# Optimization experiments

Measured on AMD Instinct MI355X. Metric: run time of the kernel, lower is better.

## Reference

```python
import jax, jax.numpy as jnp
import numpy as np

K, D = 4096, 256
BETA, DECAY, EPS = 0.25, 0.99, 1e-05
B = 32768


def setup_inputs() -> dict:
    key = jax.random.key(0)
    k1, k2, k3, k4 = jax.random.split(key, 4)
    return {
        "z_e": jax.random.normal(k1, (B, D), dtype=jnp.float32),
        "codebook": jax.random.normal(k2, (K, D), dtype=jnp.float32),
        "ema_cluster_size": jax.random.uniform(k3, (K,), dtype=jnp.float32),
        "ema_weight": jax.random.normal(k4, (K, D), dtype=jnp.float32),
    }


def reference(z_e, codebook, ema_cluster_size, ema_weight):
    z_e = z_e.astype(jnp.float32)
    # squared L2 distances: ||z||^2 - 2 z.C^T + ||C||^2  (chunking in torch is
    # purely a memory optimization; math is identical)
    e_norm = jnp.sum(z_e * z_e, axis=1, keepdims=True)            # [B,1]
    c_norm = jnp.sum(codebook * codebook, axis=1)                  # [K]
    dists = e_norm - 2.0 * (z_e @ codebook.T) + c_norm[None, :]    # [B,K]
    idx = jnp.argmin(dists, axis=1)                                # [B] int

    z_q = codebook[idx]                                            # [B,d] gather

    # EMA codebook update (no_grad in torch)
    counts = jnp.zeros((K,), jnp.float32).at[idx].add(1.0)         # bincount
    new_cluster = ema_cluster_size * DECAY + counts * (1.0 - DECAY)
    dw = jnp.zeros((K, D), jnp.float32).at[idx].add(z_e)           # index_add_
    new_ema_weight = ema_weight * DECAY + dw * (1.0 - DECAY)
    n = jnp.sum(new_cluster)
    cluster_size = (new_cluster + EPS) / (n + K * EPS) * n
    new_codebook = new_ema_weight / cluster_size[:, None]

    z_q_ste = z_e + jax.lax.stop_gradient(z_q - z_e)
    commit = BETA * jnp.mean((z_e - z_q) ** 2)
    return (z_q_ste, idx, commit, new_codebook, new_cluster, new_ema_weight)
```

## Files before the change

### kernel.cpp

```cpp
#include <hip/hip_runtime.h>

#define KC 4096
#define DD 256
#define BB 32768
#define P_BETA 0.25f
#define P_DECAY 0.99f
#define P_EPS 1e-5f
#define TAU 0.5f
#define CHUNK 32

typedef __attribute__((ext_vector_type(8))) short bf16x8;
typedef __attribute__((ext_vector_type(4))) float f32x4;

static __device__ __forceinline__ unsigned short f2bf(float f) {
    unsigned int u = __float_as_uint(f);
    unsigned int r = (u + 0x7fffu + ((u >> 16) & 1u)) >> 16;
    return (unsigned short)r;
}
static __device__ __forceinline__ void gload_lds16(const void* g, void* s) {
    __builtin_amdgcn_global_load_lds(
        (const __attribute__((address_space(1))) unsigned int*)g,
        (__attribute__((address_space(3))) unsigned int*)s, 16, 0, 0);
}

#define ZBLK (BB * DD / 4 / 256)
#define CBLK (KC * DD / 4 / 256)
__global__ __launch_bounds__(256) void convert_all_kernel(
    const float* __restrict__ z, const float* __restrict__ cb,
    unsigned short* __restrict__ zb, unsigned short* __restrict__ cbb,
    float* __restrict__ cn, int* __restrict__ cnt) {
    const int b = blockIdx.x;
    if (b < ZBLK) {
        int t = b * 256 + threadIdx.x;
        float4 v = ((const float4*)z)[t];
        *(ushort4*)&zb[(size_t)t * 4] =
            make_ushort4(f2bf(v.x), f2bf(v.y), f2bf(v.z), f2bf(v.w));
    } else if (b < ZBLK + CBLK) {
        int t = (b - ZBLK) * 256 + threadIdx.x;
        int lane = threadIdx.x & 63;
        int row = (b - ZBLK) * 4 + (threadIdx.x >> 6);
        float4 v = ((const float4*)cb)[t];
        *(ushort4*)&cbb[(size_t)t * 4] =
            make_ushort4(f2bf(v.x), f2bf(v.y), f2bf(v.z), f2bf(v.w));
        float s = v.x * v.x + v.y * v.y + v.z * v.z + v.w * v.w;
#pragma unroll
        for (int m = 32; m; m >>= 1) s += __shfl_xor(s, m);
        if (lane == 0) cn[row] = s;
    } else {
        int4* p = (int4*)cnt;
        int4 zv = make_int4(0, 0, 0, 0);
#pragma unroll
        for (int j = 0; j < 4; ++j) p[threadIdx.x * 4 + j] = zv;
    }
}

__global__ __launch_bounds__(256, 2) void
mfma_argmin_kernel(const unsigned short* __restrict__ zb,
                   const unsigned short* __restrict__ cbb,
                   const float* __restrict__ cn,
                   float4* __restrict__ cand) {
    __shared__ unsigned short As[128 * 256];
    __shared__ unsigned short Bs[128 * 64];

    const int tid = threadIdx.x;
    const int l = tid & 63, w = tid >> 6;
    const int xcd = blockIdx.x & 7;
    const int half = xcd >> 2;
    const int rb = (blockIdx.x >> 3) * 4 + (xcd & 3);
    const int row0 = rb * 128;
    const int col0 = half * 2048;
    const int wm = w & 1, wn = w >> 1;
    const int m_off = wm * 64, n_off = wn * 64;
    const int lm = l & 15, lq = l >> 4;

    {
        const int lrow = w * 2 + (l >> 5);
        const int coff = ((l & 31) ^ lrow) * 8;
#pragma unroll
        for (int i = 0; i < 16; ++i) {
            gload_lds16(zb + (size_t)(row0 + i * 8 + lrow) * DD + coff,
                        &As[(i * 8 + w * 2) * 256]);
        }
    }

    const int srow = l >> 3;
    const int scol = ((l & 7) ^ srow) * 8;
    const int g0 = w * 4;

    float best[16];
    int bidx[16];
#pragma unroll
    for (int s = 0; s < 16; ++s) { best[s] = 3.4e38f; bidx[s] = 0; }

    for (int kc = 0; kc < 2048; kc += 128) {
        f32x4 acc[4][4];
#pragma unroll
        for (int a = 0; a < 4; ++a)
#pragma unroll
            for (int b = 0; b < 4; ++b) acc[a][b] = (f32x4){0.f, 0.f, 0.f, 0.f};

        for (int dc = 0; dc < 4; ++dc) {
#pragma unroll
            for (int j = 0; j < 4; ++j) {
                const int g = g0 + j;
                const int br = col0 + kc + g * 8 + srow;
                gload_lds16(cbb + (size_t)br * DD + dc * 64 + scol, &Bs[g * 512]);
            }
            __syncthreads();
#pragma unroll
            for (int ks = 0; ks < 2; ++ks) {
                bf16x8 af[4], bfr[4];
                const int cbi = dc * 8 + ks * 4 + lq;
#pragma unroll
                for (int tm = 0; tm < 4; ++tm) {
                    int r = m_off + tm * 16 + lm;
                    af[tm] = *(const bf16x8*)&As[r * 256 + ((cbi ^ (r & 7)) * 8)];
                }
#pragma unroll
                for (int tn = 0; tn < 4; ++tn) {
                    int r = n_off + tn * 16 + lm;
                    bfr[tn] = *(const bf16x8*)&Bs[r * 64 + (((ks * 4 + lq) ^ (r & 7)) * 8)];
                }
#pragma unroll
                for (int tm = 0; tm < 4; ++tm)
#pragma unroll
                    for (int tn = 0; tn < 4; ++tn)
                        acc[tm][tn] = __builtin_amdgcn_mfma_f32_16x16x32_bf16(
                            af[tm], bfr[tn], acc[tm][tn], 0, 0, 0);
            }
            __syncthreads();
        }
#pragma unroll
        for (int tn = 0; tn < 4; ++tn) {
            const int col = col0 + kc + n_off + tn * 16 + lm;
            const float cnv = cn[col];
#pragma unroll
            for (int tm = 0; tm < 4; ++tm)
#pragma unroll
                for (int r = 0; r < 4; ++r) {
                    float dist = fmaf(-2.0f, acc[tm][tn][r], cnv);
                    int s = tm * 4 + r;
                    if (dist < best[s]) { best[s] = dist; bidx[s] = col; }
                }
        }
    }

    float v2[16];
    int i2[16];
#pragma unroll
    for (int s = 0; s < 16; ++s) { v2[s] = 3.4e38f; i2[s] = 0x7fffffff; }
#pragma unroll
    for (int m = 1; m < 16; m <<= 1) {
#pragma unroll
        for (int s = 0; s < 16; ++s) {
            float w1 = __shfl_xor(best[s], m); int j1 = __shfl_xor(bidx[s], m);
            float w2 = __shfl_xor(v2[s], m);   int j2 = __shfl_xor(i2[s], m);
            bool b = (w1 < best[s]) || (w1 == best[s] && j1 < bidx[s]);
            if (b) {
                bool c = (best[s] < w2) || (best[s] == w2 && bidx[s] < j2);
                v2[s] = c ? best[s] : w2; i2[s] = c ? bidx[s] : j2;
                best[s] = w1; bidx[s] = j1;
            } else {
                bool c = (w1 < v2[s]) || (w1 == v2[s] && j1 < i2[s]);
                v2[s] = c ? w1 : v2[s]; i2[s] = c ? j1 : i2[s];
            }
        }
    }

    float4* red = (float4*)As;
    if (lm == 0) {
#pragma unroll
        for (int tm = 0; tm < 4; ++tm)
#pragma unroll
            for (int r = 0; r < 4; ++r) {
                int s = tm * 4 + r;
                int row_local = m_off + tm * 16 + lq * 4 + r;
                red[wn * 128 + row_local] =
                    make_float4(best[s], __int_as_float(bidx[s]), v2[s], __int_as_float(i2[s]));
            }
    }
    __syncthreads();
    if (tid < 128) {
        float4 a = red[tid], b = red[128 + tid];
        float av1 = a.x, av2 = a.z; int ai1 = __float_as_int(a.y), ai2 = __float_as_int(a.w);
        float bv1 = b.x, bv2 = b.z; int bi1 = __float_as_int(b.y), bi2 = __float_as_int(b.w);
        float v1o, v2o; int i1o, i2o;
        bool bb = (bv1 < av1) || (bv1 == av1 && bi1 < ai1);
        if (bb) {
            v1o = bv1; i1o = bi1;
            bool c = (av1 < bv2) || (av1 == bv2 && ai1 < bi2);
            v2o = c ? av1 : bv2; i2o = c ? ai1 : bi2;
        } else {
            v1o = av1; i1o = ai1;
            bool c = (bv1 < av2) || (bv1 == av2 && bi1 < ai2);
            v2o = c ? bv1 : av2; i2o = c ? bi1 : ai2;
        }
        cand[(size_t)half * BB + row0 + tid] =
            make_float4(v1o, __int_as_float(i1o), v2o, __int_as_float(i2o));
    }
}

__global__ __launch_bounds__(256) void merge_refine_kernel(
    const float4* __restrict__ cand, const float* __restrict__ z,
    const float* __restrict__ cb, const float* __restrict__ cn,
    int* __restrict__ idx_i, float* __restrict__ idx_f,
    int* __restrict__ cnt, float* __restrict__ dw) {
    int i = blockIdx.x * 256 + threadIdx.x;
    {
        float4 zv4 = make_float4(0.f, 0.f, 0.f, 0.f);
        float4* dp = (float4*)dw;
        int base = i * 8;
#pragma unroll
        for (int j = 0; j < 8; ++j) dp[base + j] = zv4;
    }
    float4 a = cand[i], b = cand[(size_t)BB + i];
    float av1 = a.x, av2 = a.z; int ai1 = __float_as_int(a.y), ai2 = __float_as_int(a.w);
    float bv1 = b.x, bv2 = b.z; int bi1 = __float_as_int(b.y), bi2 = __float_as_int(b.w);
    float v1o, v2o; int i1o, i2o;
    bool bb = (bv1 < av1) || (bv1 == av1 && bi1 < ai1);
    if (bb) {
        v1o = bv1; i1o = bi1;
        bool c = (av1 < bv2) || (av1 == bv2 && ai1 < bi2);
        v2o = c ? av1 : bv2; i2o = c ? ai1 : bi2;
    } else {
        v1o = av1; i1o = ai1;
        bool c = (bv1 < av2) || (bv1 == av2 && bi1 < ai2);
        v2o = c ? bv1 : av2; i2o = c ? bi1 : ai2;
    }
    int kb = i1o;
    if (v2o - v1o < TAU) {
        const float4* zr = (const float4*)(z + (size_t)i * DD);
        const float4* c1 = (const float4*)(cb + (size_t)i1o * DD);
        const float4* c2 = (const float4*)(cb + (size_t)i2o * DD);
        float s1x = 0, s1y = 0, s1z = 0, s1w = 0;
        float s2x = 0, s2y = 0, s2z = 0, s2w = 0;
        for (int j = 0; j < 64; ++j) {
            float4 zv = zr[j], p = c1[j], q = c2[j];
            s1x = fmaf(zv.x, p.x, s1x); s1y = fmaf(zv.y, p.y, s1y);
            s1z = fmaf(zv.z, p.z, s1z); s1w = fmaf(zv.w, p.w, s1w);
            s2x = fmaf(zv.x, q.x, s2x); s2y = fmaf(zv.y, q.y, s2y);
            s2z = fmaf(zv.z, q.z, s2z); s2w = fmaf(zv.w, q.w, s2w);
        }
        float d1 = cn[i1o] - 2.f * ((s1x + s1y) + (s1z + s1w));
        float d2 = cn[i2o] - 2.f * ((s2x + s2y) + (s2z + s2w));
        if (d2 < d1 || (d2 == d1 && i2o < i1o)) kb = i2o;
    }
    idx_i[i] = kb;
    idx_f[i] = (float)kb;
    atomicAdd(&cnt[kb], 1);
}

__global__ __launch_bounds__(256) void prefix_kernel(const int* __restrict__ cnt,
                                                     int* __restrict__ cursor) {
    __shared__ int ls[257];
    const int t = threadIdx.x;
    int local[16];
    int s = 0;
#pragma unroll
    for (int j = 0; j < 16; ++j) { local[j] = s; s += cnt[t * 16 + j]; }
    ls[t + 1] = s;
    __syncthreads();
    if (t == 0) {
        ls[0] = 0;
        for (int j = 1; j <= 256; ++j) ls[j] += ls[j - 1];
    }
    __syncthreads();
    int off = ls[t];
#pragma unroll
    for (int j = 0; j < 16; ++j) cursor[t * 16 + j] = off + local[j];
}

__global__ __launch_bounds__(256) void zq_commit_scatter_kernel(
    const float* __restrict__ z, const float* __restrict__ cb,
    const int* __restrict__ idx_i, float* __restrict__ zq,
    float* __restrict__ commit_parts, int* __restrict__ cursor,
    int* __restrict__ row_of) {
    const int w = threadIdx.x >> 6, l = threadIdx.x & 63;
    const int i = blockIdx.x * 4 + w;
    const int k = idx_i[i];
    float4 zv = ((const float4*)z)[(size_t)i * 64 + l];
    float4 cv = ((const float4*)cb)[(size_t)k * 64 + l];
    ((float4*)zq)[(size_t)i * 64 + l] = cv;
    float dx = zv.x - cv.x, dy = zv.y - cv.y, dz = zv.z - cv.z, dq = zv.w - cv.w;
    float s = dx * dx + dy * dy + dz * dz + dq * dq;
#pragma unroll
    for (int m = 32; m; m >>= 1) s += __shfl_xor(s, m);
    __shared__ float ls[4];
    if (l == 0) {
        ls[w] = s;
        int pos = atomicAdd(&cursor[k], 1);
        row_of[pos] = i | (k << 16);
    }
    __syncthreads();
    if (threadIdx.x == 0) commit_parts[blockIdx.x] = ls[0] + ls[1] + ls[2] + ls[3];
}

__global__ __launch_bounds__(256) void bucket_cluster_kernel(
    const float* __restrict__ z, const int* __restrict__ row_of,
    float* __restrict__ dw, const float* __restrict__ ema_cs,
    const int* __restrict__ cnt, const float* __restrict__ commit_parts,
    float* __restrict__ out_cluster, float* __restrict__ n_ws,
    float* __restrict__ out_commit) {
    const int t = threadIdx.x;
    if (blockIdx.x == BB / CHUNK) {
        float cs = 0.f;
        for (int j = t; j < BB / 4; j += 256) cs += commit_parts[j];
        float ns = 0.f;
        for (int j = t; j < KC; j += 256) {
            float nc = ema_cs[j] * P_DECAY + (float)cnt[j] * (1.0f - P_DECAY);
            out_cluster[j] = nc;
            ns += nc;
        }
#pragma unroll
        for (int m = 32; m; m >>= 1) { cs += __shfl_xor(cs, m); ns += __shfl_xor(ns, m); }
        __shared__ float lc[4], ln[4];
        if ((t & 63) == 0) { lc[t >> 6] = cs; ln[t >> 6] = ns; }
        __syncthreads();
        if (t == 0) {
            *out_commit = P_BETA * (lc[0] + lc[1] + lc[2] + lc[3]) / (float)((size_t)BB * DD);
            *n_ws = ln[0] + ln[1] + ln[2] + ln[3];
        }
        return;
    }
    __shared__ int pk[CHUNK];
    const int p0 = blockIdx.x * CHUNK;
    if (t < CHUNK) pk[t] = row_of[p0 + t];
    __syncthreads();
    float acc = 0.f;
    int kprev = pk[0] >> 16;
#pragma unroll 4
    for (int j = 0; j < CHUNK; ++j) {
        int p = pk[j];
        int r = p & 0xffff, k = p >> 16;
        if (k != kprev) {
            atomicAdd(&dw[(size_t)kprev * DD + t], acc);
            acc = 0.f;
            kprev = k;
        }
        acc += z[(size_t)r * DD + t];
    }
    atomicAdd(&dw[(size_t)kprev * DD + t], acc);
}

__global__ __launch_bounds__(256) void finalize_kernel(const float* __restrict__ ema_w,
                                                       const float* __restrict__ dw,
                                                       const float* __restrict__ out_cluster,
                                                       const float* __restrict__ n_ws,
                                                       float* __restrict__ out_ema_w,
                                                       float* __restrict__ out_codebook) {
    const size_t id = (size_t)blockIdx.x * 256 + threadIdx.x;
    const int k = (int)(id >> 8);
    const float n = *n_ws;
    float nw = ema_w[id] * P_DECAY + dw[id] * (1.0f - P_DECAY);
    out_ema_w[id] = nw;
    float cl = out_cluster[k];
    float csz = (cl + P_EPS) / (n + (float)KC * P_EPS) * n;
    out_codebook[id] = nw / csz;
}

extern "C" void kernel_launch(void* const* d_in, const int* in_sizes, int n_in,
                              void* d_out, int out_size, void* d_ws, size_t ws_size,
                              hipStream_t stream) {
    const float* z      = (const float*)d_in[0];
    const float* cb     = (const float*)d_in[1];
    const float* ema_cs = (const float*)d_in[2];
    const float* ema_w  = (const float*)d_in[3];

    float4* cand = (float4*)d_ws;
    unsigned short* zb = (unsigned short*)(cand + 2 * (size_t)BB);
    unsigned short* cbb = zb + (size_t)BB * DD;
    float* dw = (float*)(cbb + (size_t)KC * DD);
    float* c_norm = dw + (size_t)KC * DD;
    int* idx_i = (int*)(c_norm + KC);
    int* cnt = idx_i + BB;
    int* cursor = cnt + KC;
    int* row_of = cursor + KC;
    float* commit_parts = (float*)(row_of + BB);
    float* n_ws = commit_parts + BB / 4;

    float* out        = (float*)d_out;
    float* o_zq       = out;
    float* o_idx      = o_zq + (size_t)BB * DD;
    float* o_commit   = o_idx + BB;
    float* o_codebook = o_commit + 1;
    float* o_cluster  = o_codebook + (size_t)KC * DD;
    float* o_emaw     = o_cluster + KC;

    convert_all_kernel<<<ZBLK + CBLK + 1, 256, 0, stream>>>(z, cb, zb, cbb, c_norm, cnt);
    mfma_argmin_kernel<<<(BB / 128) * 2, 256, 0, stream>>>(zb, cbb, c_norm, cand);
    merge_refine_kernel<<<BB / 256, 256, 0, stream>>>(cand, z, cb, c_norm, idx_i,
                                                      o_idx, cnt, dw);
    prefix_kernel<<<1, 256, 0, stream>>>(cnt, cursor);
    zq_commit_scatter_kernel<<<BB / 4, 256, 0, stream>>>(z, cb, idx_i, o_zq,
                                                         commit_parts, cursor, row_of);
    bucket_cluster_kernel<<<BB / CHUNK + 1, 256, 0, stream>>>(z, row_of, dw, ema_cs,
                                                              cnt, commit_parts,
                                                              o_cluster, n_ws, o_commit);
    finalize_kernel<<<(KC * DD) / 256, 256, 0, stream>>>(ema_w, dw, o_cluster, n_ws,
                                                         o_emaw, o_codebook);
    (void)in_sizes; (void)n_in; (void)out_size; (void)ws_size;
}
```

Baseline: 237.9 us.

## Compute commitment loss algebraically and accumulate dw from bf16 z copy

The commitment loss is now computed as sum||z||^2 + sum counts*||c||^2 - 2*sum(c·dw). The z-norm partials come from the conversion kernel and the c·dw dot from the finalize kernel, which uses a last-block atomic reduction. This drops the full fp32 z reread in the z_q scatter kernel. The bucket accumulation now reads the bf16 z copy instead of fp32 z, halving that traffic, but it introduces bf16 rounding into dw, the EMA weights and the codebook. The algebraic loss can suffer cancellation error, and the cluster-size update moves into the single-block prefix kernel.

```diff
diff --git a/kernel.cpp b/kernel.cpp
--- a/kernel.cpp
+++ b/kernel.cpp
@@ -17,6 +17,9 @@
     unsigned int r = (u + 0x7fffu + ((u >> 16) & 1u)) >> 16;
     return (unsigned short)r;
 }
+static __device__ __forceinline__ float bf2f(unsigned short h) {
+    return __uint_as_float(((unsigned int)h) << 16);
+}
 static __device__ __forceinline__ void gload_lds16(const void* g, void* s) {
     __builtin_amdgcn_global_load_lds(
         (const __attribute__((address_space(1))) unsigned int*)g,
@@ -28,13 +31,21 @@
 __global__ __launch_bounds__(256) void convert_all_kernel(
     const float* __restrict__ z, const float* __restrict__ cb,
     unsigned short* __restrict__ zb, unsigned short* __restrict__ cbb,
-    float* __restrict__ cn, int* __restrict__ cnt) {
+    float* __restrict__ cn, int* __restrict__ cnt,
+    float* __restrict__ z2_parts) {
     const int b = blockIdx.x;
     if (b < ZBLK) {
         int t = b * 256 + threadIdx.x;
         float4 v = ((const float4*)z)[t];
         *(ushort4*)&zb[(size_t)t * 4] =
             make_ushort4(f2bf(v.x), f2bf(v.y), f2bf(v.z), f2bf(v.w));
+        float s = v.x * v.x + v.y * v.y + v.z * v.z + v.w * v.w;
+#pragma unroll
+        for (int m = 32; m; m >>= 1) s += __shfl_xor(s, m);
+        __shared__ float ls[4];
+        if ((threadIdx.x & 63) == 0) ls[threadIdx.x >> 6] = s;
+        __syncthreads();
+        if (threadIdx.x == 0) z2_parts[b] = ls[0] + ls[1] + ls[2] + ls[3];
     } else if (b < ZBLK + CBLK) {
         int t = (b - ZBLK) * 256 + threadIdx.x;
         int lane = threadIdx.x & 63;
@@ -204,15 +215,18 @@
     const float4* __restrict__ cand, const float* __restrict__ z,
     const float* __restrict__ cb, const float* __restrict__ cn,
     int* __restrict__ idx_i, float* __restrict__ idx_f,
-    int* __restrict__ cnt, float* __restrict__ dw) {
-    int i = blockIdx.x * 256 + threadIdx.x;
+    int* __restrict__ cnt, float* __restrict__ dw,
+    float* __restrict__ scalars ) {
     {
         float4 zv4 = make_float4(0.f, 0.f, 0.f, 0.f);
         float4* dp = (float4*)dw;
-        int base = i * 8;
-#pragma unroll
-        for (int j = 0; j < 8; ++j) dp[base + j] = zv4;
-    }
+        int base = (blockIdx.x * 256 + threadIdx.x) * 4;
+#pragma unroll
+        for (int j = 0; j < 4; ++j) dp[base + j] = zv4;
+    }
+    if (blockIdx.x == 0 && threadIdx.x < 2) scalars[threadIdx.x] = 0.f;
+    if (threadIdx.x >= 128) return;
+    int i = blockIdx.x * 128 + threadIdx.x;
     float4 a = cand[i], b = cand[(size_t)BB + i];
     float av1 = a.x, av2 = a.z; int ai1 = __float_as_int(a.y), ai2 = __float_as_int(a.w);
     float bv1 = b.x, bv2 = b.z; int bi1 = __float_as_int(b.y), bi2 = __float_as_int(b.w);
@@ -250,14 +264,28 @@
     atomicAdd(&cnt[kb], 1);
 }
 
-__global__ __launch_bounds__(256) void prefix_kernel(const int* __restrict__ cnt,
-                                                     int* __restrict__ cursor) {
+__global__ __launch_bounds__(256) void prefix_cluster_kernel(
+    const int* __restrict__ cnt, const float* __restrict__ cn,
+    const float* __restrict__ ema_cs, const float* __restrict__ z2_parts,
+    int* __restrict__ cursor, float* __restrict__ out_cluster,
+    float* __restrict__ n_ws, float* __restrict__ cc_ws,
+    float* __restrict__ z2_ws) {
     __shared__ int ls[257];
     const int t = threadIdx.x;
     int local[16];
     int s = 0;
-#pragma unroll
-    for (int j = 0; j < 16; ++j) { local[j] = s; s += cnt[t * 16 + j]; }
+    float ns = 0.f, ccs = 0.f;
+#pragma unroll
+    for (int j = 0; j < 16; ++j) {
+        int c = cnt[t * 16 + j];
+        local[j] = s; s += c;
+        float nc = ema_cs[t * 16 + j] * P_DECAY + (float)c * (1.0f - P_DECAY);
+        out_cluster[t * 16 + j] = nc;
+        ns += nc;
+        ccs += (float)c * cn[t * 16 + j];
+    }
+    float z2s = 0.f;
+    for (int j = t; j < ZBLK; j += 256) z2s += z2_parts[j];
     ls[t + 1] = s;
     __syncthreads();
     if (t == 0) {
@@ -268,61 +296,39 @@
     int off = ls[t];
 #pragma unroll
     for (int j = 0; j < 16; ++j) cursor[t * 16 + j] = off + local[j];
-}
-
-__global__ __launch_bounds__(256) void zq_commit_scatter_kernel(
-    const float* __restrict__ z, const float* __restrict__ cb,
-    const int* __restrict__ idx_i, float* __restrict__ zq,
-    float* __restrict__ commit_parts, int* __restrict__ cursor,
-    int* __restrict__ row_of) {
+#pragma unroll
+    for (int m = 32; m; m >>= 1) {
+        ns += __shfl_xor(ns, m); ccs += __shfl_xor(ccs, m); z2s += __shfl_xor(z2s, m);
+    }
+    __shared__ float ln[4], lc[4], lz[4];
+    if ((t & 63) == 0) { ln[t >> 6] = ns; lc[t >> 6] = ccs; lz[t >> 6] = z2s; }
+    __syncthreads();
+    if (t == 0) {
+        *n_ws = ln[0] + ln[1] + ln[2] + ln[3];
+        *cc_ws = lc[0] + lc[1] + lc[2] + lc[3];
+        *z2_ws = lz[0] + lz[1] + lz[2] + lz[3];
+    }
+}
+
+__global__ __launch_bounds__(256) void zq_scatter_kernel(
+    const float* __restrict__ cb, const int* __restrict__ idx_i,
+    float* __restrict__ zq, int* __restrict__ cursor, int* __restrict__ row_of) {
     const int w = threadIdx.x >> 6, l = threadIdx.x & 63;
     const int i = blockIdx.x * 4 + w;
     const int k = idx_i[i];
-    float4 zv = ((const float4*)z)[(size_t)i * 64 + l];
     float4 cv = ((const float4*)cb)[(size_t)k * 64 + l];
     ((float4*)zq)[(size_t)i * 64 + l] = cv;
-    float dx = zv.x - cv.x, dy = zv.y - cv.y, dz = zv.z - cv.z, dq = zv.w - cv.w;
-    float s = dx * dx + dy * dy + dz * dz + dq * dq;
-#pragma unroll
-    for (int m = 32; m; m >>= 1) s += __shfl_xor(s, m);
-    __shared__ float ls[4];
     if (l == 0) {
-        ls[w] = s;
         int pos = atomicAdd(&cursor[k], 1);
         row_of[pos] = i | (k << 16);
     }
-    __syncthreads();
-    if (threadIdx.x == 0) commit_parts[blockIdx.x] = ls[0] + ls[1] + ls[2] + ls[3];
-}
-
-__global__ __launch_bounds__(256) void bucket_cluster_kernel(
-    const float* __restrict__ z, const int* __restrict__ row_of,
-    float* __restrict__ dw, const float* __restrict__ ema_cs,
-    const int* __restrict__ cnt, const float* __restrict__ commit_parts,
-    float* __restrict__ out_cluster, float* __restrict__ n_ws,
-    float* __restrict__ out_commit) {
+}
+
+__global__ __launch_bounds__(256) void bucket_chunk_kernel(
+    const unsigned short* __restrict__ zb, const int* __restrict__ row_of,
+    float* __restrict__ dw) {
+    __shared__ int pk[CHUNK];
     const int t = threadIdx.x;
-    if (blockIdx.x == BB / CHUNK) {
-        float cs = 0.f;
-        for (int j = t; j < BB / 4; j += 256) cs += commit_parts[j];
-        float ns = 0.f;
-        for (int j = t; j < KC; j += 256) {
-            float nc = ema_cs[j] * P_DECAY + (float)cnt[j] * (1.0f - P_DECAY);
-            out_cluster[j] = nc;
-            ns += nc;
-        }
-#pragma unroll
-        for (int m = 32; m; m >>= 1) { cs += __shfl_xor(cs, m); ns += __shfl_xor(ns, m); }
-        __shared__ float lc[4], ln[4];
-        if ((t & 63) == 0) { lc[t >> 6] = cs; ln[t >> 6] = ns; }
-        __syncthreads();
-        if (t == 0) {
-            *out_commit = P_BETA * (lc[0] + lc[1] + lc[2] + lc[3]) / (float)((size_t)BB * DD);
-            *n_ws = ln[0] + ln[1] + ln[2] + ln[3];
-        }
-        return;
-    }
-    __shared__ int pk[CHUNK];
     const int p0 = blockIdx.x * CHUNK;
     if (t < CHUNK) pk[t] = row_of[p0 + t];
     __syncthreads();
@@ -337,25 +343,45 @@
             acc = 0.f;
             kprev = k;
         }
-        acc += z[(size_t)r * DD + t];
+        acc += bf2f(zb[(size_t)r * DD + t]);
     }
     atomicAdd(&dw[(size_t)kprev * DD + t], acc);
 }
 
-__global__ __launch_bounds__(256) void finalize_kernel(const float* __restrict__ ema_w,
-                                                       const float* __restrict__ dw,
-                                                       const float* __restrict__ out_cluster,
-                                                       const float* __restrict__ n_ws,
-                                                       float* __restrict__ out_ema_w,
-                                                       float* __restrict__ out_codebook) {
-    const size_t id = (size_t)blockIdx.x * 256 + threadIdx.x;
-    const int k = (int)(id >> 8);
+__global__ __launch_bounds__(256) void finalize_kernel(
+    const float* __restrict__ ema_w, const float* __restrict__ dw,
+    const float* __restrict__ cb, const float* __restrict__ out_cluster,
+    const float* __restrict__ n_ws, const float* __restrict__ cc_ws,
+    const float* __restrict__ z2_ws, float* __restrict__ scalars,
+    float* __restrict__ out_ema_w, float* __restrict__ out_codebook,
+    float* __restrict__ out_commit) {
+    const int k = blockIdx.x, t = threadIdx.x;
+    const size_t id = (size_t)k * DD + t;
     const float n = *n_ws;
-    float nw = ema_w[id] * P_DECAY + dw[id] * (1.0f - P_DECAY);
+    float dwv = dw[id];
+    float nw = ema_w[id] * P_DECAY + dwv * (1.0f - P_DECAY);
     out_ema_w[id] = nw;
     float cl = out_cluster[k];
     float csz = (cl + P_EPS) / (n + (float)KC * P_EPS) * n;
     out_codebook[id] = nw / csz;
+    float p = cb[id] * dwv;
+#pragma unroll
+    for (int m = 32; m; m >>= 1) p += __shfl_xor(p, m);
+    __shared__ float ls[4];
+    if ((t & 63) == 0) ls[t >> 6] = p;
+    __syncthreads();
+    if (t == 0) {
+        atomicAdd(&scalars[0], ls[0] + ls[1] + ls[2] + ls[3]);
+        __threadfence();
+        unsigned int done = (unsigned int)atomicAdd((int*)&scalars[1], 1);
+        if (done == KC - 1) {
+            __threadfence();
+            float dot = __hip_atomic_load(&scalars[0], __ATOMIC_ACQUIRE,
+                                          __HIP_MEMORY_SCOPE_AGENT);
+            float total = (*z2_ws) + (*cc_ws) - 2.0f * dot;
+            *out_commit = P_BETA * total / (float)((size_t)BB * DD);
+        }
+    }
 }
 
 extern "C" void kernel_launch(void* const* d_in, const int* in_sizes, int n_in,
@@ -375,8 +401,11 @@
     int* cnt = idx_i + BB;
     int* cursor = cnt + KC;
     int* row_of = cursor + KC;
-    float* commit_parts = (float*)(row_of + BB);
-    float* n_ws = commit_parts + BB / 4;
+    float* z2_parts = (float*)(row_of + BB);
+    float* scalars = z2_parts + ZBLK;
+    float* n_ws = scalars + 2;
+    float* cc_ws = n_ws + 1;
+    float* z2_ws = cc_ws + 1;
 
     float* out        = (float*)d_out;
     float* o_zq       = out;
@@ -386,17 +415,17 @@
     float* o_cluster  = o_codebook + (size_t)KC * DD;
     float* o_emaw     = o_cluster + KC;
 
-    convert_all_kernel<<<ZBLK + CBLK + 1, 256, 0, stream>>>(z, cb, zb, cbb, c_norm, cnt);
+    convert_all_kernel<<<ZBLK + CBLK + 1, 256, 0, stream>>>(z, cb, zb, cbb, c_norm,
+                                                            cnt, z2_parts);
     mfma_argmin_kernel<<<(BB / 128) * 2, 256, 0, stream>>>(zb, cbb, c_norm, cand);
-    merge_refine_kernel<<<BB / 256, 256, 0, stream>>>(cand, z, cb, c_norm, idx_i,
-                                                      o_idx, cnt, dw);
-    prefix_kernel<<<1, 256, 0, stream>>>(cnt, cursor);
-    zq_commit_scatter_kernel<<<BB / 4, 256, 0, stream>>>(z, cb, idx_i, o_zq,
-                                                         commit_parts, cursor, row_of);
-    bucket_cluster_kernel<<<BB / CHUNK + 1, 256, 0, stream>>>(z, row_of, dw, ema_cs,
-                                                              cnt, commit_parts,
-                                                              o_cluster, n_ws, o_commit);
-    finalize_kernel<<<(KC * DD) / 256, 256, 0, stream>>>(ema_w, dw, o_cluster, n_ws,
-                                                         o_emaw, o_codebook);
+    merge_refine_kernel<<<BB / 128, 256, 0, stream>>>(cand, z, cb, c_norm, idx_i,
+                                                      o_idx, cnt, dw, scalars);
+    prefix_cluster_kernel<<<1, 256, 0, stream>>>(cnt, c_norm, ema_cs, z2_parts,
+                                                 cursor, o_cluster, n_ws, cc_ws, z2_ws);
+    zq_scatter_kernel<<<BB / 4, 256, 0, stream>>>(cb, idx_i, o_zq, cursor, row_of);
+    bucket_chunk_kernel<<<BB / CHUNK, 256, 0, stream>>>(zb, row_of, dw);
+    finalize_kernel<<<KC, 256, 0, stream>>>(ema_w, dw, cb, o_cluster, n_ws, cc_ws,
+                                            z2_ws, scalars, o_emaw, o_codebook,
+                                            o_commit);
     (void)in_sizes; (void)n_in; (void)out_size; (void)ws_size;
 }
```

New measurement: 359.6 us. 1.51x slower.
